# Kernel tuning notes

Measured on AMD Instinct MI355X. Metric: run time of the kernel, lower is better.

The kernel has to match this reference:

```python
import jax, jax.numpy as jnp
import numpy as np

TEMPERATURE = 0.5
EPS = 1e-12  # F.normalize eps


def setup_inputs() -> dict:
    key = jax.random.key(0)
    z = jax.random.normal(key, (2048, 8, 256), dtype=jnp.float32)
    return {"z": z}


def reference(z):
    B, D = z.shape[0], z.shape[1]
    z = z.reshape(B, D, -1)  # [B, D, F]
    # F.normalize along features
    norm = jnp.linalg.norm(z, axis=-1, keepdims=True)
    zn = z / jnp.maximum(norm, EPS)

    # Positive term: per sample b, sim among D views -> [B, D, D], off-diagonal sum
    sim_pos = jnp.exp(jnp.einsum('bdf,bef->bde', zn, zn) / TEMPERATURE)
    eye_d = jnp.eye(D, dtype=bool)
    pos = jnp.sum(jnp.where(eye_d[None], 0.0, sim_pos), axis=(1, 2))  # [B]

    # Negative term: per view d, sim among B samples -> [D, B, B], row-wise off-diag mean, summed over views
    sim_neg = jnp.exp(jnp.einsum('bdf,cdf->dbc', zn, zn) / TEMPERATURE)
    eye_b = jnp.eye(B, dtype=bool)
    neg = jnp.sum(jnp.where(eye_b[None], 0.0, sim_neg), axis=-1) / (B - 1)  # [D, B]
    neg = jnp.sum(neg, axis=0)  # [B]

    logits = pos / (pos + neg)  # [B]
    # torch CrossEntropyLoss(reduction='sum') with 1-D input [C] and float target ones(C):
    # loss = -sum_c target_c * log_softmax(logits)_c = -sum(log_softmax(logits))
    error = -jnp.sum(jax.nn.log_softmax(logits))
    return error / B
```

## Files before the change

kernel.cpp:

```cpp
#include <hip/hip_runtime.h>
#include <hip/hip_bf16.h>

#define B_N 2048
#define D_V 8
#define F_D 256
#define TILE 128
#define BC 64
#define LSTR 264

#define SCALE_F 1.69864364f

#if defined(__has_builtin)
#  if __has_builtin(__builtin_amdgcn_exp2f)
#    define EXP2F(x) __builtin_amdgcn_exp2f(x)
#  else
#    define EXP2F(x) exp2f(x)
#  endif
#else
#  define EXP2F(x) exp2f(x)
#endif

typedef __attribute__((ext_vector_type(8))) short short8;
typedef __attribute__((ext_vector_type(4))) float floatx4;

__device__ inline unsigned short f2bf(float f) {
    __hip_bfloat16 h = __float2bfloat16(f);
    return *reinterpret_cast<unsigned short*>(&h);
}

__device__ inline float wave_reduce_sum(float v) {
    #pragma unroll
    for (int off = 1; off < 64; off <<= 1)
        v += __shfl_xor(v, off, 64);
    return v;
}

__global__ void norm_kernel(const float* __restrict__ z,
                            unsigned short* __restrict__ zn,
                            float* __restrict__ ns8) {
    int gid = blockIdx.x * blockDim.x + threadIdx.x;
    if (gid < D_V * B_N) ns8[gid] = 0.0f;
    int wave = gid >> 6;
    int lane = threadIdx.x & 63;
    const float4* zp = (const float4*)(z + (size_t)wave * F_D);
    float4 v = zp[lane];
    float ss = v.x * v.x + v.y * v.y + v.z * v.z + v.w * v.w;
    ss = wave_reduce_sum(ss);
    float inv = SCALE_F / fmaxf(sqrtf(ss), 1e-12f);
    int b = wave >> 3, d = wave & 7;
    unsigned short* op = zn + (size_t)d * (B_N * F_D) + (size_t)b * F_D + lane * 4;
    ushort4 o;
    o.x = f2bf(v.x * inv);
    o.y = f2bf(v.y * inv);
    o.z = f2bf(v.z * inv);
    o.w = f2bf(v.w * inv);
    *(ushort4*)op = o;
}

__global__ void pos_kernel(const unsigned short* __restrict__ zn,
                           float* __restrict__ pos) {
    int gw = (blockIdx.x * blockDim.x + threadIdx.x) >> 6;
    int lane = threadIdx.x & 63;
    int q = lane >> 4, li = lane & 15;
    int s0 = gw * 2;
    int b = s0 + (li >> 3), d = li & 7;
    const unsigned short* rowp = zn + (size_t)d * (B_N * F_D) + (size_t)b * F_D;
    short8 a[8];
    #pragma unroll
    for (int kk = 0; kk < 8; kk++)
        a[kk] = *(const short8*)(rowp + kk * 32 + q * 8);
    floatx4 acc = {0.f, 0.f, 0.f, 0.f};
    #pragma unroll
    for (int kk = 0; kk < 8; kk++)
        acc = __builtin_amdgcn_mfma_f32_16x16x32_bf16(a[kk], a[kk], acc, 0, 0, 0);
    float p0 = 0.f, p1 = 0.f;
    #pragma unroll
    for (int r = 0; r < 4; r++) {
        int row = q * 4 + r, col = li;
        bool same_sample = (row >> 3) == (col >> 3);
        if (same_sample && row != col) {
            float e = EXP2F(acc[r]);
            if (row < 8) p0 += e; else p1 += e;
        }
    }
    p0 = wave_reduce_sum(p0);
    p1 = wave_reduce_sum(p1);
    if (lane == 0) { pos[s0] = p0; pos[s0 + 1] = p1; }
}

__global__ __launch_bounds__(256)
void neg_kernel(const unsigned short* __restrict__ zn,
                float* __restrict__ ns8) {
    __shared__ __align__(16) unsigned short Bs[BC * LSTR];
    const int bid = blockIdx.x;
    const int d = bid & 7;
    int trem = bid >> 3;
    int i = 0;
    while (trem >= 16 - i) { trem -= 16 - i; ++i; }
    const int j = i + trem;
    const bool diag = (i == j);
    const unsigned short* Z = zn + (size_t)d * (B_N * F_D);
    int tid = threadIdx.x, w = tid >> 6, lane = tid & 63;
    int q = lane >> 4, li = lane & 15;
    int r0 = i * TILE + w * 32;

    short8 a[2][8];
    #pragma unroll
    for (int s = 0; s < 2; s++)
        #pragma unroll
        for (int kk = 0; kk < 8; kk++)
            a[s][kk] = *(const short8*)(Z + (size_t)(r0 + s * 16 + li) * F_D + kk * 32 + q * 8);

    float rs[2][4];
    #pragma unroll
    for (int s = 0; s < 2; s++)
        #pragma unroll
        for (int r = 0; r < 4; r++) rs[s][r] = 0.f;
    float cs[8];

    #pragma unroll
    for (int stage = 0; stage < 2; ++stage) {
        int c0 = j * TILE + stage * BC;
        __syncthreads();
        #pragma unroll
        for (int it = 0; it < 8; ++it) {
            int idx = it * 256 + tid;
            int row = idx >> 5, kc = idx & 31;
            *(short8*)(&Bs[row * LSTR + kc * 8]) =
                *(const short8*)(Z + (size_t)(c0 + row) * F_D + kc * 8);
        }
        __syncthreads();
        #pragma unroll
        for (int ct = 0; ct < 4; ++ct) {
            const unsigned short* bp = &Bs[(ct * 16 + li) * LSTR + q * 8];
            floatx4 acc[2];
            acc[0] = (floatx4){0.f, 0.f, 0.f, 0.f};
            acc[1] = (floatx4){0.f, 0.f, 0.f, 0.f};
            #pragma unroll
            for (int kk = 0; kk < 8; kk++) {
                short8 bf = *(const short8*)(bp + kk * 32);
                acc[0] = __builtin_amdgcn_mfma_f32_16x16x32_bf16(a[0][kk], bf, acc[0], 0, 0, 0);
                acc[1] = __builtin_amdgcn_mfma_f32_16x16x32_bf16(a[1][kk], bf, acc[1], 0, 0, 0);
            }
            int gcol = c0 + ct * 16 + li;
            float csum = 0.f;
            #pragma unroll
            for (int s = 0; s < 2; s++) {
                #pragma unroll
                for (int r = 0; r < 4; r++) {
                    float e = EXP2F(acc[s][r]);
                    if (diag) {
                        int grow = r0 + s * 16 + q * 4 + r;
                        if (grow == gcol) e = 0.f;
                    }
                    rs[s][r] += e;
                    csum += e;
                }
            }
            cs[stage * 4 + ct] = csum;
        }
    }

    #pragma unroll
    for (int off = 1; off < 16; off <<= 1)
        #pragma unroll
        for (int s = 0; s < 2; s++)
            #pragma unroll
            for (int r = 0; r < 4; r++)
                rs[s][r] += __shfl_xor(rs[s][r], off, 64);
    {
        float rv = 0.f;
        #pragma unroll
        for (int s = 0; s < 2; s++)
            #pragma unroll
            for (int r = 0; r < 4; r++)
                if (li == s * 4 + r) rv = rs[s][r];
        if (li < 8)
            atomicAdd(&ns8[d * B_N + r0 + (li >> 2) * 16 + q * 4 + (li & 3)], rv);
    }

    if (!diag) {
        #pragma unroll
        for (int c = 0; c < 8; c++) {
            cs[c] += __shfl_xor(cs[c], 16, 64);
            cs[c] += __shfl_xor(cs[c], 32, 64);
        }
        float v0 = 0.f, v1 = 0.f;
        #pragma unroll
        for (int c = 0; c < 4; c++)
            if (q == c) { v0 = cs[c]; v1 = cs[c + 4]; }
        atomicAdd(&ns8[d * B_N + j * TILE + q * 16 + li], v0);
        atomicAdd(&ns8[d * B_N + j * TILE + 64 + q * 16 + li], v1);
    }
}

__global__ void final_kernel(const float* __restrict__ pos,
                             const float* __restrict__ ns8,
                             float* __restrict__ out) {
    __shared__ float red[256];
    int t = threadIdx.x;
    float vals[8];
    float lmax = -1e30f;
    #pragma unroll
    for (int i = 0; i < 8; i++) {
        int idx = t * 8 + i;
        float nsum = 0.f;
        #pragma unroll
        for (int d = 0; d < D_V; d++) nsum += ns8[d * B_N + idx];
        float p = pos[idx];
        float n = nsum * (1.0f / (float)(B_N - 1));
        float l = p / (p + n);
        vals[i] = l;
        lmax = fmaxf(lmax, l);
    }
    red[t] = lmax; __syncthreads();
    for (int s = 128; s > 0; s >>= 1) {
        if (t < s) red[t] = fmaxf(red[t], red[t + s]);
        __syncthreads();
    }
    float m = red[0]; __syncthreads();
    float se = 0.f, sl = 0.f;
    #pragma unroll
    for (int i = 0; i < 8; i++) { se += expf(vals[i] - m); sl += vals[i]; }
    red[t] = se; __syncthreads();
    for (int s = 128; s > 0; s >>= 1) {
        if (t < s) red[t] += red[t + s];
        __syncthreads();
    }
    float S = red[0]; __syncthreads();
    red[t] = sl; __syncthreads();
    for (int s = 128; s > 0; s >>= 1) {
        if (t < s) red[t] += red[t + s];
        __syncthreads();
    }
    if (t == 0) out[0] = m + logf(S) - red[0] / (float)B_N;
}

extern "C" void kernel_launch(void* const* d_in, const int* in_sizes, int n_in,
                              void* d_out, int out_size, void* d_ws, size_t ws_size,
                              hipStream_t stream) {
    const float* z = (const float*)d_in[0];
    float* out = (float*)d_out;
    unsigned short* zn = (unsigned short*)d_ws;
    float* ns8 = (float*)((char*)d_ws + (size_t)D_V * B_N * F_D * 2);
    float* pos = ns8 + D_V * B_N;

    norm_kernel<<<dim3(4096), 256, 0, stream>>>(z, zn, ns8);
    pos_kernel<<<dim3(256), 256, 0, stream>>>(zn, pos);
    neg_kernel<<<dim3(136 * 8), 256, 0, stream>>>(zn, ns8);
    final_kernel<<<1, 256, 0, stream>>>(pos, ns8, out);
}
```

Measured before the change: 95.09 us.

## Fuse normalize and positive-term kernels, prefetch second B stage into registers

Merges the normalization and positive-similarity kernels into one kernel. Each block normalizes 4 samples, stages them in shared memory and computes the positive term from LDS rather than re-reading global memory, which removes one launch and a pass over zn. The negative kernel now prefetches the second 64-row B chunk into registers while the first chunk is being consumed, overlapping global loads with MFMA work. It also sets launch_bounds to 2 blocks per CU. This raises register pressure through the breg buffer, and the fused kernel has fewer blocks with half its waves idle during the positive phase.

```diff
diff --git a/kernel.cpp b/kernel.cpp
--- a/kernel.cpp
+++ b/kernel.cpp
@@ -35,60 +35,97 @@
     return v;
 }
 
-__global__ void norm_kernel(const float* __restrict__ z,
-                            unsigned short* __restrict__ zn,
-                            float* __restrict__ ns8) {
-    int gid = blockIdx.x * blockDim.x + threadIdx.x;
+__global__ __launch_bounds__(256)
+void np_kernel(const float* __restrict__ z, unsigned short* __restrict__ zn,
+               float* __restrict__ ns8, float* __restrict__ pos) {
+    __shared__ __align__(16) unsigned short Zs[32 * LSTR];
+    int tid = threadIdx.x;
+    int gid = blockIdx.x * 256 + tid;
     if (gid < D_V * B_N) ns8[gid] = 0.0f;
-    int wave = gid >> 6;
-    int lane = threadIdx.x & 63;
-    const float4* zp = (const float4*)(z + (size_t)wave * F_D);
-    float4 v = zp[lane];
-    float ss = v.x * v.x + v.y * v.y + v.z * v.z + v.w * v.w;
-    ss = wave_reduce_sum(ss);
-    float inv = SCALE_F / fmaxf(sqrtf(ss), 1e-12f);
-    int b = wave >> 3, d = wave & 7;
-    unsigned short* op = zn + (size_t)d * (B_N * F_D) + (size_t)b * F_D + lane * 4;
-    ushort4 o;
-    o.x = f2bf(v.x * inv);
-    o.y = f2bf(v.y * inv);
-    o.z = f2bf(v.z * inv);
-    o.w = f2bf(v.w * inv);
-    *(ushort4*)op = o;
-}
-
-__global__ void pos_kernel(const unsigned short* __restrict__ zn,
-                           float* __restrict__ pos) {
-    int gw = (blockIdx.x * blockDim.x + threadIdx.x) >> 6;
-    int lane = threadIdx.x & 63;
-    int q = lane >> 4, li = lane & 15;
-    int s0 = gw * 2;
-    int b = s0 + (li >> 3), d = li & 7;
-    const unsigned short* rowp = zn + (size_t)d * (B_N * F_D) + (size_t)b * F_D;
-    short8 a[8];
-    #pragma unroll
-    for (int kk = 0; kk < 8; kk++)
-        a[kk] = *(const short8*)(rowp + kk * 32 + q * 8);
-    floatx4 acc = {0.f, 0.f, 0.f, 0.f};
-    #pragma unroll
-    for (int kk = 0; kk < 8; kk++)
-        acc = __builtin_amdgcn_mfma_f32_16x16x32_bf16(a[kk], a[kk], acc, 0, 0, 0);
-    float p0 = 0.f, p1 = 0.f;
-    #pragma unroll
-    for (int r = 0; r < 4; r++) {
-        int row = q * 4 + r, col = li;
-        bool same_sample = (row >> 3) == (col >> 3);
-        if (same_sample && row != col) {
-            float e = EXP2F(acc[r]);
-            if (row < 8) p0 += e; else p1 += e;
+
+    int w = tid >> 6, lane = tid & 63;
+    int b = blockIdx.x * 4 + w;
+    #pragma unroll
+    for (int k = 0; k < 8; k++) {
+        const float4 v = ((const float4*)(z + ((size_t)b * 8 + k) * F_D))[lane];
+        float ss = v.x * v.x + v.y * v.y + v.z * v.z + v.w * v.w;
+        ss = wave_reduce_sum(ss);
+        float inv = SCALE_F / fmaxf(sqrtf(ss), 1e-12f);
+        ushort4 o;
+        o.x = f2bf(v.x * inv);
+        o.y = f2bf(v.y * inv);
+        o.z = f2bf(v.z * inv);
+        o.w = f2bf(v.w * inv);
+        ((ushort4*)(zn + (size_t)k * (B_N * F_D) + (size_t)b * F_D))[lane] = o;
+        *(ushort4*)(&Zs[(w * 8 + k) * LSTR + lane * 4]) = o;
+    }
+    __syncthreads();
+
+    if (w < 2) {
+        int q = lane >> 4, li = lane & 15;
+        int lr = (w * 2 + (li >> 3)) * 8 + (li & 7);
+        short8 a[8];
+        #pragma unroll
+        for (int kk = 0; kk < 8; kk++)
+            a[kk] = *(const short8*)(&Zs[lr * LSTR + kk * 32 + q * 8]);
+        floatx4 acc = {0.f, 0.f, 0.f, 0.f};
+        #pragma unroll
+        for (int kk = 0; kk < 8; kk++)
+            acc = __builtin_amdgcn_mfma_f32_16x16x32_bf16(a[kk], a[kk], acc, 0, 0, 0);
+        float p0 = 0.f, p1 = 0.f;
+        #pragma unroll
+        for (int r = 0; r < 4; r++) {
+            int row = q * 4 + r, col = li;
+            bool same_sample = (row >> 3) == (col >> 3);
+            if (same_sample && row != col) {
+                float e = EXP2F(acc[r]);
+                if (row < 8) p0 += e; else p1 += e;
+            }
         }
-    }
-    p0 = wave_reduce_sum(p0);
-    p1 = wave_reduce_sum(p1);
-    if (lane == 0) { pos[s0] = p0; pos[s0 + 1] = p1; }
-}
-
-__global__ __launch_bounds__(256)
+        p0 = wave_reduce_sum(p0);
+        p1 = wave_reduce_sum(p1);
+        if (lane == 0) {
+            int s0 = blockIdx.x * 4 + w * 2;
+            pos[s0] = p0;
+            pos[s0 + 1] = p1;
+        }
+    }
+}
+
+#define CT_SWEEP(C0, CSB)                                                        \
+    do {                                                                         \
+        _Pragma("unroll")                                                        \
+        for (int ct = 0; ct < 4; ++ct) {                                         \
+            const unsigned short* bp = &Bs[(ct * 16 + li) * LSTR + q * 8];       \
+            floatx4 acc[2];                                                      \
+            acc[0] = (floatx4){0.f, 0.f, 0.f, 0.f};                              \
+            acc[1] = (floatx4){0.f, 0.f, 0.f, 0.f};                              \
+            _Pragma("unroll")                                                    \
+            for (int kk = 0; kk < 8; kk++) {                                     \
+                short8 bf = *(const short8*)(bp + kk * 32);                      \
+                acc[0] = __builtin_amdgcn_mfma_f32_16x16x32_bf16(a[0][kk], bf, acc[0], 0, 0, 0); \
+                acc[1] = __builtin_amdgcn_mfma_f32_16x16x32_bf16(a[1][kk], bf, acc[1], 0, 0, 0); \
+            }                                                                    \
+            int gcol = (C0) + ct * 16 + li;                                      \
+            float csum = 0.f;                                                    \
+            _Pragma("unroll")                                                    \
+            for (int s = 0; s < 2; s++) {                                        \
+                _Pragma("unroll")                                                \
+                for (int r = 0; r < 4; r++) {                                    \
+                    float e = EXP2F(acc[s][r]);                                  \
+                    if (diag) {                                                  \
+                        int grow = r0 + s * 16 + q * 4 + r;                      \
+                        if (grow == gcol) e = 0.f;                               \
+                    }                                                            \
+                    rs[s][r] += e;                                               \
+                    csum += e;                                                   \
+                }                                                                \
+            }                                                                    \
+            cs[(CSB) + ct] = csum;                                               \
+        }                                                                        \
+    } while (0)
+
+__global__ __launch_bounds__(256, 2)
 void neg_kernel(const unsigned short* __restrict__ zn,
                 float* __restrict__ ns8) {
     __shared__ __align__(16) unsigned short Bs[BC * LSTR];
@@ -111,6 +148,27 @@
         for (int kk = 0; kk < 8; kk++)
             a[s][kk] = *(const short8*)(Z + (size_t)(r0 + s * 16 + li) * F_D + kk * 32 + q * 8);
 
+    int brow = 0, bkc = 0;
+    short8 breg[8];
+    #pragma unroll
+    for (int it = 0; it < 8; ++it) {
+        int idx = it * 256 + tid;
+        int row = idx >> 5, kc = idx & 31;
+        breg[it] = *(const short8*)(Z + (size_t)(j * TILE + row) * F_D + kc * 8);
+    }
+    #pragma unroll
+    for (int it = 0; it < 8; ++it) {
+        int idx = it * 256 + tid;
+        int row = idx >> 5, kc = idx & 31;
+        *(short8*)(&Bs[row * LSTR + kc * 8]) = breg[it];
+    }
+    #pragma unroll
+    for (int it = 0; it < 8; ++it) {
+        int idx = it * 256 + tid;
+        int row = idx >> 5, kc = idx & 31;
+        breg[it] = *(const short8*)(Z + (size_t)(j * TILE + BC + row) * F_D + kc * 8);
+    }
+
     float rs[2][4];
     #pragma unroll
     for (int s = 0; s < 2; s++)
@@ -118,48 +176,17 @@
         for (int r = 0; r < 4; r++) rs[s][r] = 0.f;
     float cs[8];
 
-    #pragma unroll
-    for (int stage = 0; stage < 2; ++stage) {
-        int c0 = j * TILE + stage * BC;
-        __syncthreads();
-        #pragma unroll
-        for (int it = 0; it < 8; ++it) {
-            int idx = it * 256 + tid;
-            int row = idx >> 5, kc = idx & 31;
-            *(short8*)(&Bs[row * LSTR + kc * 8]) =
-                *(const short8*)(Z + (size_t)(c0 + row) * F_D + kc * 8);
-        }
-        __syncthreads();
-        #pragma unroll
-        for (int ct = 0; ct < 4; ++ct) {
-            const unsigned short* bp = &Bs[(ct * 16 + li) * LSTR + q * 8];
-            floatx4 acc[2];
-            acc[0] = (floatx4){0.f, 0.f, 0.f, 0.f};
-            acc[1] = (floatx4){0.f, 0.f, 0.f, 0.f};
-            #pragma unroll
-            for (int kk = 0; kk < 8; kk++) {
-                short8 bf = *(const short8*)(bp + kk * 32);
-                acc[0] = __builtin_amdgcn_mfma_f32_16x16x32_bf16(a[0][kk], bf, acc[0], 0, 0, 0);
-                acc[1] = __builtin_amdgcn_mfma_f32_16x16x32_bf16(a[1][kk], bf, acc[1], 0, 0, 0);
-            }
-            int gcol = c0 + ct * 16 + li;
-            float csum = 0.f;
-            #pragma unroll
-            for (int s = 0; s < 2; s++) {
-                #pragma unroll
-                for (int r = 0; r < 4; r++) {
-                    float e = EXP2F(acc[s][r]);
-                    if (diag) {
-                        int grow = r0 + s * 16 + q * 4 + r;
-                        if (grow == gcol) e = 0.f;
-                    }
-                    rs[s][r] += e;
-                    csum += e;
-                }
-            }
-            cs[stage * 4 + ct] = csum;
-        }
-    }
+    __syncthreads();
+    CT_SWEEP(j * TILE, 0);
+    __syncthreads();
+    #pragma unroll
+    for (int it = 0; it < 8; ++it) {
+        int idx = it * 256 + tid;
+        int row = idx >> 5, kc = idx & 31;
+        *(short8*)(&Bs[row * LSTR + kc * 8]) = breg[it];
+    }
+    __syncthreads();
+    CT_SWEEP(j * TILE + BC, 4);
 
     #pragma unroll
     for (int off = 1; off < 16; off <<= 1)
@@ -245,8 +272,7 @@
     float* ns8 = (float*)((char*)d_ws + (size_t)D_V * B_N * F_D * 2);
     float* pos = ns8 + D_V * B_N;
 
-    norm_kernel<<<dim3(4096), 256, 0, stream>>>(z, zn, ns8);
-    pos_kernel<<<dim3(256), 256, 0, stream>>>(zn, pos);
+    np_kernel<<<dim3(512), 256, 0, stream>>>(z, zn, ns8, pos);
     neg_kernel<<<dim3(136 * 8), 256, 0, stream>>>(zn, ns8);
     final_kernel<<<1, 256, 0, stream>>>(pos, ns8, out);
 }
```

Result: faster. 86.27 us (-9.3%).
